# Kernel tuning notes

Hardware: AMD Instinct MI355X
Metric: run time of the kernel (lower is better)

Reference implementation:

```python
import jax, jax.numpy as jnp
import numpy as np

N = 10000   # nodes
E = 160000  # edges
IN_DIM, HID, OUT_DIM = 512, 512, 256


def setup_inputs() -> dict:
    key = jax.random.key(0)
    ks = jax.random.split(key, 10)
    x = jax.random.normal(ks[0], (N, IN_DIM), dtype=jnp.float32)
    edge_index = jax.random.randint(ks[1], (2, E), 0, N, dtype=jnp.int32)
    s = 0.05
    return {
        "x": x,
        "edge_index": edge_index,
        # GIN inner MLP (iVAE-style MLP with n_layers=1 == single Linear)
        "f_W": jax.random.normal(ks[2], (IN_DIM, HID), jnp.float32) * s,
        "f_b": jnp.zeros((HID,), jnp.float32),
        # GCNConv linear
        "gcn_W": jax.random.normal(ks[3], (IN_DIM + HID, OUT_DIM), jnp.float32) * s,
        "gcn_b": jnp.zeros((OUT_DIM,), jnp.float32),
        # decode MLP: out_dim -> out_dim/2 -> 2 with relu between
        "d1_W": jax.random.normal(ks[4], (OUT_DIM, OUT_DIM // 2), jnp.float32) * s,
        "d1_b": jnp.zeros((OUT_DIM // 2,), jnp.float32),
        "d2_W": jax.random.normal(ks[5], (OUT_DIM // 2, 2), jnp.float32) * s,
        "d2_b": jnp.zeros((2,), jnp.float32),
    }


def reference(x, edge_index, f_W, f_b, gcn_W, gcn_b, d1_W, d1_b, d2_W, d2_b):
    src, dst = edge_index[0], edge_index[1]

    # ---- GINConv(f, eps=-1.0): out = f((1+eps)*x + sum_{j in N(i)} x_j)
    # eps = -1 => (1+eps) = 0, so only the neighbor sum survives.
    agg = jax.ops.segment_sum(x[src], dst, num_segments=N)      # [N, in_dim]
    h1 = agg @ f_W + f_b                                        # [N, hid]

    # (the original computes z1 = (h1-mean)/std when regularize=True, but it is
    #  overwritten before being returned -> dead code, skipped)

    # ---- GCNConv on cat(x, h1) with self-loops + symmetric normalization
    xh = jnp.concatenate((x, h1), axis=1)                       # [N, in+hid]
    h = xh @ gcn_W                                              # [N, out]

    loop = jnp.arange(N, dtype=src.dtype)
    src_f = jnp.concatenate([src, loop])                        # [E+N]
    dst_f = jnp.concatenate([dst, loop])
    deg = jax.ops.segment_sum(jnp.ones_like(dst_f, jnp.float32), dst_f,
                              num_segments=N)                   # [N]
    dis = jnp.where(deg > 0, jax.lax.rsqrt(jnp.maximum(deg, 1.0)), 0.0)
    norm = dis[src_f] * dis[dst_f]                              # [E+N]
    out = jax.ops.segment_sum(h[src_f] * norm[:, None], dst_f,
                              num_segments=N) + gcn_b           # [N, out]

    # ---- decode MLP: Linear -> relu -> Linear
    z = jax.nn.relu(out @ d1_W + d1_b)
    z1 = z @ d2_W + d2_b                                        # [N, 2]
    return z1
```

## Files before the change

kernel.cpp:

```cpp
#include <hip/hip_runtime.h>

#define N_NODES 10000
#define E_EDGES 160000
#define IN_DIM  512
#define HID_DIM 512
#define OUT_DIM 256
#define MB_T    157

typedef __attribute__((ext_vector_type(8))) short short8;
typedef __attribute__((ext_vector_type(16))) float f32x16;
typedef unsigned short u16;

__device__ __forceinline__ u16 f2bh(float f) {
  union { float f; unsigned u; } v; v.f = f;
  return (u16)((v.u + 0x7FFFu + ((v.u >> 16) & 1u)) >> 16);
}
__device__ __forceinline__ float bh2f(u16 h) {
  union { unsigned u; float f; } v; v.u = ((unsigned)h) << 16;
  return v.f;
}

__device__ __forceinline__ size_t tidx(int mb, int ktTot, int kt, int c) {
  return ((size_t)(mb * ktTot + kt) * 256 + c) * 8;
}
__device__ __forceinline__ short8 g16(const u16* p) {
  return *reinterpret_cast<const short8*>(p);
}

#define GL_LDS(gsrc, ldst)                                                      \
  __builtin_amdgcn_global_load_lds(                                             \
      (const __attribute__((address_space(1))) unsigned int*)(gsrc),            \
      (__attribute__((address_space(3))) unsigned int*)(ldst), 16, 0, 0)

__global__ __launch_bounds__(1024) void scan_kernel(
    int* __restrict__ cnt, int* __restrict__ row, float* __restrict__ dis) {
  __shared__ int wsum[16];
  const int CH = 10;
  int t = threadIdx.x;
  int lane = t & 63, wid = t >> 6;
  int c[CH], excl[CH];
  int s = 0;
#pragma unroll
  for (int j = 0; j < CH; ++j) {
    int idx = t * CH + j;
    c[j] = (idx < N_NODES) ? cnt[idx] : 0;
    excl[j] = s;
    s += c[j];
  }
  int incl = s;
#pragma unroll
  for (int off = 1; off < 64; off <<= 1) {
    int v = __shfl_up(incl, off);
    if (lane >= off) incl += v;
  }
  if (lane == 63) wsum[wid] = incl;
  __syncthreads();
  if (t < 16) {
    int v = wsum[t];
#pragma unroll
    for (int off = 1; off < 16; off <<= 1) {
      int u = __shfl_up(v, off);
      if (t >= off) v += u;
    }
    wsum[t] = v;
  }
  __syncthreads();
  int waveBase = (wid == 0) ? 0 : wsum[wid - 1];
  int base = waveBase + incl - s;
#pragma unroll
  for (int j = 0; j < CH; ++j) {
    int idx = t * CH + j;
    if (idx < N_NODES) {
      int start = base + excl[j];
      row[idx] = start;
      cnt[idx] = start;
      dis[idx] = rsqrtf((float)c[j] + 1.0f);
    }
  }
  if (t == 1023) row[N_NODES] = wsum[15];
}

#define PREP_PACKX  5000
#define PREP_PACKFW 5256
#define PREP_CONVT  5320
#define PREP_C2END  5336
#define PREP_TOTAL  5961

__device__ __forceinline__ void pack_row(const float* __restrict__ src,
                                         u16* __restrict__ hi, u16* __restrict__ lo,
                                         int i, int tt) {
  int k0 = tt * 4;
  float4 v = *reinterpret_cast<const float4*>(src + (size_t)i * 512 + k0);
  float a[4] = {v.x, v.y, v.z, v.w};
  ushort4 h4, l4;
  u16* hp = &h4.x; u16* lp = &l4.x;
#pragma unroll
  for (int j = 0; j < 4; ++j) {
    u16 hh = f2bh(a[j]);
    hp[j] = hh;
    lp[j] = f2bh(a[j] - bh2f(hh));
  }
  int mb = i >> 6, rl = i & 63;
  int kt = k0 >> 5, si = (k0 >> 4) & 1, kh = (k0 >> 3) & 1;
  int c = (rl >> 5) * 128 + si * 64 + kh * 32 + (rl & 31);
  size_t idx = tidx(mb, 16, kt, c) + (k0 & 7);
  *reinterpret_cast<ushort4*>(hi + idx) = h4;
  *reinterpret_cast<ushort4*>(lo + idx) = l4;
}

__global__ __launch_bounds__(256) void prep_kernel(
    const float* __restrict__ x, const float* __restrict__ f_W,
    const float* __restrict__ gcn_W, const float* __restrict__ f_b,
    const int* __restrict__ dst, int* __restrict__ icnt,
    u16* __restrict__ x_hi, u16* __restrict__ x_lo,
    u16* __restrict__ fWp_hi, u16* __restrict__ fWp_lo,
    u16* __restrict__ Wcomb_hi, u16* __restrict__ Wcomb_lo,
    u16* __restrict__ WbotT_hi, u16* __restrict__ WbotT_lo,
    float* __restrict__ c2) {
  __shared__ float tile[64][65];
  int b = blockIdx.x, t = threadIdx.x;

  if (b < PREP_PACKX) {
    int i = b * 2 + (t >> 7);
    pack_row(x, x_hi, x_lo, i, t & 127);
  } else if (b < PREP_PACKFW) {
    int i = (b - PREP_PACKX) * 2 + (t >> 7);
    pack_row(f_W, fWp_hi, fWp_lo, i, t & 127);
  } else if (b < PREP_CONVT) {
    int lb = b - PREP_PACKFW;
    int part = lb >> 5;
    int li = lb & 31;
    int k0g = (li >> 2) * 64;
    int n0 = (li & 3) * 64;
    const float* W = part ? (gcn_W + (size_t)IN_DIM * OUT_DIM) : gcn_W;
    u16* hi = part ? WbotT_hi : Wcomb_hi;
    u16* lo = part ? WbotT_lo : Wcomb_lo;
    int lk = t >> 4, ln = (t & 15) * 4;
#pragma unroll
    for (int p = 0; p < 4; ++p) {
      float4 v = *reinterpret_cast<const float4*>(W + (size_t)(k0g + p * 16 + lk) * 256 + n0 + ln);
      tile[p * 16 + lk][ln + 0] = v.x;
      tile[p * 16 + lk][ln + 1] = v.y;
      tile[p * 16 + lk][ln + 2] = v.z;
      tile[p * 16 + lk][ln + 3] = v.w;
    }
    __syncthreads();
    int on = t >> 2;
    int ok = (t & 3) * 16;
    int colg = n0 + on;
    int nb = colg >> 6, rl = colg & 63;
#pragma unroll
    for (int q = 0; q < 4; ++q) {
      int kg = k0g + ok + q * 4;
      ushort4 h4, l4;
      u16* hq = &h4.x; u16* lq = &l4.x;
#pragma unroll
      for (int j = 0; j < 4; ++j) {
        float v = tile[ok + q * 4 + j][on];
        u16 hh = f2bh(v);
        hq[j] = hh;
        lq[j] = f2bh(v - bh2f(hh));
      }
      int kt = kg >> 5, si = (kg >> 4) & 1, kh = (kg >> 3) & 1;
      int c = (rl >> 5) * 128 + si * 64 + kh * 32 + (rl & 31);
      size_t idx = tidx(nb, 16, kt, c) + (kg & 7);
      *reinterpret_cast<ushort4*>(hi + idx) = h4;
      *reinterpret_cast<ushort4*>(lo + idx) = l4;
    }
  } else if (b < PREP_C2END) {
    int cb = b - PREP_CONVT;
    float s = 0.f;
    int kb = cb * 32;
#pragma unroll 8
    for (int k = kb; k < kb + 32; ++k)
      s += f_b[k] * gcn_W[(size_t)(IN_DIM + k) * OUT_DIM + t];
    atomicAdd(&c2[t], s);
  } else {
    int e = (b - PREP_C2END) * 256 + t;
    if (e < E_EDGES) atomicAdd(&icnt[dst[e]], 1);
  }
}

#define PW_PLACE 625
#define PW_TOTAL 657

__global__ __launch_bounds__(256) void pw_kernel(
    const int* __restrict__ src, const int* __restrict__ dst,
    int* __restrict__ cursor, int* __restrict__ col,
    const u16* __restrict__ WbotT_hi, const u16* __restrict__ WbotT_lo,
    const u16* __restrict__ fWp_hi, const u16* __restrict__ fWp_lo,
    u16* __restrict__ Wcomb_hi, u16* __restrict__ Wcomb_lo) {
  __shared__ u16 H[8192];
  int b = blockIdx.x, t = threadIdx.x;

  if (b < PW_PLACE) {
    int e = b * 256 + t;
    if (e < E_EDGES) {
      int pos = atomicAdd(&cursor[dst[e]], 1);
      col[pos] = src[e];
    }
    return;
  }

  int lb = b - PW_PLACE;
  int nb = lb & 7;
  int mbw = lb >> 3;
  int w = t >> 6, l = t & 63;
  int wr = w >> 1, wc = w & 1;
  int cA = wr * 128 + l;
  int cB = wc * 128 + l;

  f32x16 acc0, acc1;
#pragma unroll
  for (int r = 0; r < 16; ++r) { acc0[r] = 0.f; acc1[r] = 0.f; }

#define W2LOAD(KT, AH0, AL0, BH0, BL0, AH1, AL1, BH1, BL1)                     \
  {                                                                            \
    size_t a0 = tidx(mbw, 16, (KT), cA);                                       \
    size_t a1 = tidx(mbw, 16, (KT), cA + 64);                                  \
    size_t b0 = tidx(nb, 16, (KT), cB);                                        \
    size_t b1 = tidx(nb, 16, (KT), cB + 64);                                   \
    AH0 = g16(WbotT_hi + a0); AL0 = g16(WbotT_lo + a0);                        \
    BH0 = g16(fWp_hi + b0);   BL0 = g16(fWp_lo + b0);                          \
    AH1 = g16(WbotT_hi + a1); AL1 = g16(WbotT_lo + a1);                        \
    BH1 = g16(fWp_hi + b1);   BL1 = g16(fWp_lo + b1);                          \
  }
#define W2MMA(AH0, AL0, BH0, BL0, AH1, AL1, BH1, BL1)                          \
  {                                                                            \
    acc0 = __builtin_amdgcn_mfma_f32_32x32x16_bf16(AH0, BH0, acc0, 0, 0, 0);   \
    acc0 = __builtin_amdgcn_mfma_f32_32x32x16_bf16(AL0, BH0, acc0, 0, 0, 0);   \
    acc0 = __builtin_amdgcn_mfma_f32_32x32x16_bf16(AH0, BL0, acc0, 0, 0, 0);   \
    acc1 = __builtin_amdgcn_mfma_f32_32x32x16_bf16(AH1, BH1, acc1, 0, 0, 0);   \
    acc1 = __builtin_amdgcn_mfma_f32_32x32x16_bf16(AL1, BH1, acc1, 0, 0, 0);   \
    acc1 = __builtin_amdgcn_mfma_f32_32x32x16_bf16(AH1, BL1, acc1, 0, 0, 0);   \
  }

  short8 xah0, xal0, xbh0, xbl0, xah1, xal1, xbh1, xbl1;
  short8 yah0, yal0, ybh0, ybl0, yah1, yal1, ybh1, ybl1;
  W2LOAD(0, xah0, xal0, xbh0, xbl0, xah1, xal1, xbh1, xbl1)
#pragma unroll
  for (int kt = 0; kt < 16; kt += 2) {
    W2LOAD(kt + 1, yah0, yal0, ybh0, ybl0, yah1, yal1, ybh1, ybl1)
    W2MMA(xah0, xal0, xbh0, xbl0, xah1, xal1, xbh1, xbl1)
    if (kt + 2 < 16)
      W2LOAD(kt + 2, xah0, xal0, xbh0, xbl0, xah1, xal1, xbh1, xbl1)
    W2MMA(yah0, yal0, ybh0, ybl0, yah1, yal1, ybh1, ybl1)
  }
#undef W2LOAD
#undef W2MMA

  f32x16 acc = acc0 + acc1;
  u16* Hhi = H;
  u16* Hlo = H + 4096;
  int r0l = wr * 32 + 4 * (l >> 5);
  int c0l = wc * 32 + (l & 31);
#pragma unroll
  for (int r = 0; r < 16; ++r) {
    int rl = r0l + (r & 3) + 8 * (r >> 2);
    float v = acc[r];
    u16 hh = f2bh(v);
    Hhi[rl * 64 + c0l] = hh;
    Hlo[rl * 64 + c0l] = f2bh(v - bh2f(hh));
  }
  __syncthreads();
#pragma unroll
  for (int pl = 0; pl < 2; ++pl) {
    const u16* Hs = pl ? Hlo : Hhi;
    u16* dA = pl ? Wcomb_lo : Wcomb_hi;
#pragma unroll
    for (int j = 0; j < 2; ++j) {
      int ci = t + j * 256;
      int ktl = ci >> 8;
      int c = ci & 255;
      int r = ((c >> 7) & 1) * 32 + (c & 31);
      int kloc = ktl * 32 + ((c >> 6) & 1) * 16 + ((c >> 5) & 1) * 8;
      short8 v = *reinterpret_cast<const short8*>(Hs + r * 64 + kloc);
      size_t db = tidx(mbw + 4, 16, nb * 2 + ktl, c);
      *reinterpret_cast<short8*>(dA + db) = v;
    }
  }
}

template <int NB>
__global__ __launch_bounds__(256) void zgemm_kernel(
    const u16* __restrict__ Ah, const u16* __restrict__ Al,
    const u16* __restrict__ Bh, const u16* __restrict__ Bl,
    float* __restrict__ z1, u16* __restrict__ z2b, int M, int K) {
  constexpr int BCH = NB * 256;
  __shared__ short8 S[2][512 + 2 * BCH];

  int bid = blockIdx.x;
  int X = bid & 7, sslot = bid >> 3;
  int mb = X + 8 * (sslot >> 2);
  int nbB = sslot & 3;
  if (mb >= MB_T) return;

  int t = threadIdx.x, w = t >> 6, l = t & 63;
  int wr = w >> 1, wc = w & 1;
  int cid = t;
  int ktTot = K >> 5;

  f32x16 acc[NB][2];
#pragma unroll
  for (int n = 0; n < NB; ++n)
#pragma unroll
    for (int si = 0; si < 2; ++si)
#pragma unroll
      for (int r = 0; r < 16; ++r) acc[n][si][r] = 0.f;

  int nt = K / 32;

#define ZSTAGE(BUF, K0)                                                        \
  {                                                                            \
    size_t ab = tidx(mb, ktTot, (K0) >> 5, cid);                               \
    short8* base = &S[BUF][0] + w * 64;                                        \
    GL_LDS(Ah + ab, base);                                                     \
    GL_LDS(Al + ab, base + 256);                                               \
    _Pragma("unroll") for (int j = 0; j < NB; ++j) {                           \
      size_t bb = tidx(nbB * NB + j, ktTot, (K0) >> 5, cid);                   \
      GL_LDS(Bh + bb, base + 512 + j * 256);                                   \
      GL_LDS(Bl + bb, base + 512 + BCH + j * 256);                             \
    }                                                                          \
  }

  ZSTAGE(0, 0)
  for (int ti = 0; ti < nt; ++ti) {
    int b = ti & 1;
    __syncthreads();
    if (ti + 1 < nt) ZSTAGE(b ^ 1, (ti + 1) * 32)
#pragma unroll
    for (int si = 0; si < 2; ++si) {
      short8 ah = S[b][wr * 128 + si * 64 + l];
      short8 al = S[b][256 + wr * 128 + si * 64 + l];
#pragma unroll
      for (int n2 = 0; n2 < NB; ++n2) {
        short8 bh = S[b][512 + wc * 256 + n2 * 128 + si * 64 + l];
        short8 bl = S[b][512 + BCH + wc * 256 + n2 * 128 + si * 64 + l];
        acc[n2][si] = __builtin_amdgcn_mfma_f32_32x32x16_bf16(ah, bh, acc[n2][si], 0, 0, 0);
        acc[n2][si] = __builtin_amdgcn_mfma_f32_32x32x16_bf16(al, bh, acc[n2][si], 0, 0, 0);
        acc[n2][si] = __builtin_amdgcn_mfma_f32_32x32x16_bf16(ah, bl, acc[n2][si], 0, 0, 0);
      }
    }
  }
#undef ZSTAGE

  int r0 = mb * 64 + wr * 32 + 4 * (l >> 5);
#pragma unroll
  for (int n2 = 0; n2 < NB; ++n2) {
    f32x16 a = acc[n2][0] + acc[n2][1];
    int colg = nbB * (NB * 64) + wc * 64 + n2 * 32 + (l & 31);
#pragma unroll
    for (int r = 0; r < 16; ++r) {
      int rowg = r0 + (r & 3) + 8 * (r >> 2);
      if (rowg < M) {
        float v = a[r];
        if (colg < 256) z1[(size_t)rowg * 256 + colg] = v;
        else            z2b[(size_t)rowg * 256 + colg - 256] = f2bh(v);
      }
    }
  }
}

__global__ __launch_bounds__(128) void h_build_kernel(
    const float* __restrict__ z1, const u16* __restrict__ z2b,
    const int* __restrict__ row, const int* __restrict__ col,
    const float* __restrict__ c2, float* __restrict__ h,
    u16* __restrict__ h_bf) {
  int i = blockIdx.x * 2 + (threadIdx.x >> 6);
  int t = threadIdx.x & 63;
  int half = t >> 5, sl = t & 31;
  int beg = row[i], end = row[i + 1];

  float a0[8] = {}, a1[8] = {}, a2[8] = {}, a3[8] = {};
  int e = beg + half;
  for (; e + 6 < end; e += 8) {
    int s0 = col[e], s1 = col[e + 2], s2 = col[e + 4], s3 = col[e + 6];
    short8 v0 = *reinterpret_cast<const short8*>(z2b + (size_t)s0 * 256 + sl * 8);
    short8 v1 = *reinterpret_cast<const short8*>(z2b + (size_t)s1 * 256 + sl * 8);
    short8 v2 = *reinterpret_cast<const short8*>(z2b + (size_t)s2 * 256 + sl * 8);
    short8 v3 = *reinterpret_cast<const short8*>(z2b + (size_t)s3 * 256 + sl * 8);
#pragma unroll
    for (int j = 0; j < 8; ++j) {
      a0[j] += bh2f((u16)v0[j]);
      a1[j] += bh2f((u16)v1[j]);
      a2[j] += bh2f((u16)v2[j]);
      a3[j] += bh2f((u16)v3[j]);
    }
  }
  for (; e < end; e += 2) {
    int s = col[e];
    short8 v = *reinterpret_cast<const short8*>(z2b + (size_t)s * 256 + sl * 8);
#pragma unroll
    for (int j = 0; j < 8; ++j) a0[j] += bh2f((u16)v[j]);
  }
  float acc[8];
#pragma unroll
  for (int j = 0; j < 8; ++j) {
    acc[j] = a0[j] + a1[j] + a2[j] + a3[j];
    acc[j] += __shfl_xor(acc[j], 32);
  }
  float4 z1a = *reinterpret_cast<const float4*>(z1 + (size_t)i * 256 + sl * 8);
  float4 z1b = *reinterpret_cast<const float4*>(z1 + (size_t)i * 256 + sl * 8 + 4);
  float4 ca = *reinterpret_cast<const float4*>(c2 + sl * 8);
  float4 cb = *reinterpret_cast<const float4*>(c2 + sl * 8 + 4);
  float hv[8] = {z1a.x + ca.x + acc[0], z1a.y + ca.y + acc[1],
                 z1a.z + ca.z + acc[2], z1a.w + ca.w + acc[3],
                 z1b.x + cb.x + acc[4], z1b.y + cb.y + acc[5],
                 z1b.z + cb.z + acc[6], z1b.w + cb.w + acc[7]};
  if (half == 0) {
    float4 o0{hv[0], hv[1], hv[2], hv[3]};
    float4 o1{hv[4], hv[5], hv[6], hv[7]};
    *reinterpret_cast<float4*>(h + (size_t)i * 256 + sl * 8) = o0;
    *reinterpret_cast<float4*>(h + (size_t)i * 256 + sl * 8 + 4) = o1;
    short8 hb;
#pragma unroll
    for (int j = 0; j < 8; ++j) hb[j] = (short)f2bh(hv[j]);
    *reinterpret_cast<short8*>(h_bf + (size_t)i * 256 + sl * 8) = hb;
  }
}

__global__ __launch_bounds__(128) void gcn_gather_kernel(
    const float* __restrict__ h, const u16* __restrict__ h_bf,
    const int* __restrict__ row, const int* __restrict__ col,
    const float* __restrict__ dis, const float* __restrict__ gcn_b,
    float* __restrict__ outg) {
  int i = blockIdx.x * 2 + (threadIdx.x >> 6);
  int t = threadIdx.x & 63;
  int half = t >> 5, sl = t & 31;
  int beg = row[i], end = row[i + 1];
  float di = dis[i];

  float a0[8] = {}, a1[8] = {}, a2[8] = {}, a3[8] = {};
  int e = beg + half;
  for (; e + 6 < end; e += 8) {
    int s0 = col[e], s1 = col[e + 2], s2 = col[e + 4], s3 = col[e + 6];
    float w0 = dis[s0], w1 = dis[s1], w2 = dis[s2], w3 = dis[s3];
    short8 v0 = *reinterpret_cast<const short8*>(h_bf + (size_t)s0 * 256 + sl * 8);
    short8 v1 = *reinterpret_cast<const short8*>(h_bf + (size_t)s1 * 256 + sl * 8);
    short8 v2 = *reinterpret_cast<const short8*>(h_bf + (size_t)s2 * 256 + sl * 8);
    short8 v3 = *reinterpret_cast<const short8*>(h_bf + (size_t)s3 * 256 + sl * 8);
#pragma unroll
    for (int j = 0; j < 8; ++j) {
      a0[j] += w0 * bh2f((u16)v0[j]);
      a1[j] += w1 * bh2f((u16)v1[j]);
      a2[j] += w2 * bh2f((u16)v2[j]);
      a3[j] += w3 * bh2f((u16)v3[j]);
    }
  }
  for (; e < end; e += 2) {
    int s = col[e];
    float wv = dis[s];
    short8 v = *reinterpret_cast<const short8*>(h_bf + (size_t)s * 256 + sl * 8);
#pragma unroll
    for (int j = 0; j < 8; ++j) a0[j] += wv * bh2f((u16)v[j]);
  }
  float acc[8];
#pragma unroll
  for (int j = 0; j < 8; ++j) {
    acc[j] = a0[j] + a1[j] + a2[j] + a3[j];
    acc[j] += __shfl_xor(acc[j], 32);
  }
  if (half == 0) {
    float4 ha = *reinterpret_cast<const float4*>(h + (size_t)i * 256 + sl * 8);
    float4 hb = *reinterpret_cast<const float4*>(h + (size_t)i * 256 + sl * 8 + 4);
    float4 ba = *reinterpret_cast<const float4*>(gcn_b + sl * 8);
    float4 bb = *reinterpret_cast<const float4*>(gcn_b + sl * 8 + 4);
    float self = di * di;
    float4 o0{di * acc[0] + self * ha.x + ba.x, di * acc[1] + self * ha.y + ba.y,
              di * acc[2] + self * ha.z + ba.z, di * acc[3] + self * ha.w + ba.w};
    float4 o1{di * acc[4] + self * hb.x + bb.x, di * acc[5] + self * hb.y + bb.y,
              di * acc[6] + self * hb.z + bb.z, di * acc[7] + self * hb.w + bb.w};
    *reinterpret_cast<float4*>(outg + (size_t)i * 256 + sl * 8) = o0;
    *reinterpret_cast<float4*>(outg + (size_t)i * 256 + sl * 8 + 4) = o1;
  }
}

#define DEC_NODES 8
__global__ __launch_bounds__(128) void decode_kernel(
    const float* __restrict__ outg, const float* __restrict__ d1_W,
    const float* __restrict__ d1_b, const float* __restrict__ d2_W,
    const float* __restrict__ d2_b, float* __restrict__ z1) {
  __shared__ float rows[DEC_NODES][OUT_DIM];
  __shared__ float s0[128], s1[128];
  int t = threadIdx.x;
  int n0 = blockIdx.x * DEC_NODES;
#pragma unroll
  for (int j = 0; j < 4; ++j) {
    int idx = j * 512 + t * 4;
    *reinterpret_cast<float4*>(&rows[0][idx]) =
        *reinterpret_cast<const float4*>(outg + (size_t)n0 * OUT_DIM + idx);
  }
  __syncthreads();
  float acc[DEC_NODES];
  float b1 = d1_b[t];
#pragma unroll
  for (int n = 0; n < DEC_NODES; ++n) acc[n] = b1;
#pragma unroll 4
  for (int k = 0; k < OUT_DIM; ++k) {
    float wv = d1_W[k * 128 + t];
#pragma unroll
    for (int n = 0; n < DEC_NODES; ++n) acc[n] += rows[n][k] * wv;
  }
  float w0 = d2_W[t * 2 + 0], w1 = d2_W[t * 2 + 1];
  for (int n = 0; n < DEC_NODES; ++n) {
    float a = fmaxf(acc[n], 0.f);
    s0[t] = a * w0;
    s1[t] = a * w1;
    __syncthreads();
    for (int off = 64; off > 0; off >>= 1) {
      if (t < off) {
        s0[t] += s0[t + off];
        s1[t] += s1[t + off];
      }
      __syncthreads();
    }
    if (t == 0) {
      z1[(size_t)(n0 + n) * 2 + 0] = s0[0] + d2_b[0];
      z1[(size_t)(n0 + n) * 2 + 1] = s1[0] + d2_b[1];
    }
    __syncthreads();
  }
}

extern "C" void kernel_launch(void* const* d_in, const int* in_sizes, int n_in,
                              void* d_out, int out_size, void* d_ws, size_t ws_size,
                              hipStream_t stream) {
  const float* x     = (const float*)d_in[0];
  const int*   edge  = (const int*)d_in[1];
  const float* f_W   = (const float*)d_in[2];
  const float* f_b   = (const float*)d_in[3];
  const float* gcn_W = (const float*)d_in[4];
  const float* gcn_b = (const float*)d_in[5];
  const float* d1_W  = (const float*)d_in[6];
  const float* d1_b  = (const float*)d_in[7];
  const float* d2_W  = (const float*)d_in[8];
  const float* d2_b  = (const float*)d_in[9];
  float* out = (float*)d_out;
  char*  wsb = (char*)d_ws;

  const int* src = edge;
  const int* dst = edge + E_EDGES;

  const size_t TS   = (size_t)MB_T * 16 * 256 * 8 * sizeof(u16);
  const size_t WTLE = (size_t)16 * 256 * 8 * sizeof(u16);

  size_t o = 0;
  u16*   x_hi = (u16*)(wsb + o); o += TS;
  u16*   x_lo = (u16*)(wsb + o); o += TS;
  float* z1   = (float*)(wsb + o); o += (size_t)N_NODES * 256 * 4;
  u16*   z2b  = (u16*)(wsb + o);   o += (size_t)N_NODES * 256 * 2;
  float* h    = (float*)(wsb + o); o += (size_t)N_NODES * 256 * 4;
  u16*   h_bf = (u16*)(wsb + o);   o += (size_t)N_NODES * 256 * 2;
  float* dis8 = (float*)(wsb + o); o += (size_t)N_NODES * 4;
  int*   icnt8 = (int*)(wsb + o);  o += (size_t)N_NODES * 4;
  float* c2   = (float*)(wsb + o); o += OUT_DIM * 4;
  int*   irow8 = (int*)(wsb + o);  o += (size_t)(N_NODES + 1) * 4 + 12;
  int*   icol8 = (int*)(wsb + o);  o += (size_t)E_EDGES * 4;
  u16*   Wcomb_hi = (u16*)(wsb + o); o += 8 * WTLE;
  u16*   Wcomb_lo = (u16*)(wsb + o); o += 8 * WTLE;
  u16*   WbotT_hi = (u16*)(wsb + o); o += 4 * WTLE;
  u16*   WbotT_lo = (u16*)(wsb + o); o += 4 * WTLE;
  u16*   fWp_hi   = (u16*)(wsb + o); o += 8 * WTLE;
  u16*   fWp_lo   = (u16*)(wsb + o); o += 8 * WTLE;
  float* outg = (float*)(wsb + 0);
  const size_t v8_needed = o;

  if (ws_size >= v8_needed) {
    hipMemsetAsync(icnt8, 0, (size_t)N_NODES * sizeof(int) + OUT_DIM * sizeof(float), stream);

    prep_kernel<<<PREP_TOTAL, 256, 0, stream>>>(
        x, f_W, gcn_W, f_b, dst, icnt8, x_hi, x_lo, fWp_hi, fWp_lo,
        Wcomb_hi, Wcomb_lo, WbotT_hi, WbotT_lo, c2);

    scan_kernel<<<1, 1024, 0, stream>>>(icnt8, irow8, dis8);

    pw_kernel<<<PW_TOTAL, 256, 0, stream>>>(
        src, dst, icnt8, icol8, WbotT_hi, WbotT_lo, fWp_hi, fWp_lo,
        Wcomb_hi, Wcomb_lo);

    zgemm_kernel<2><<<640, 256, 0, stream>>>(
        x_hi, x_lo, Wcomb_hi, Wcomb_lo, z1, z2b, N_NODES, IN_DIM);

    h_build_kernel<<<N_NODES / 2, 128, 0, stream>>>(z1, z2b, irow8, icol8, c2, h, h_bf);

    gcn_gather_kernel<<<N_NODES / 2, 128, 0, stream>>>(h, h_bf, irow8, icol8, dis8, gcn_b, outg);
    decode_kernel<<<N_NODES / DEC_NODES, 128, 0, stream>>>(outg, d1_W, d1_b, d2_W, d2_b, out);
  }
}
```

Baseline: 142.5 us.

## Split bf16 gather tables into column halves for L2-resident neighbor gathers

```diff
diff --git a/kernel.cpp b/kernel.cpp
--- a/kernel.cpp
+++ b/kernel.cpp
@@ -285,7 +285,8 @@
 __global__ __launch_bounds__(256) void zgemm_kernel(
     const u16* __restrict__ Ah, const u16* __restrict__ Al,
     const u16* __restrict__ Bh, const u16* __restrict__ Bl,
-    float* __restrict__ z1, u16* __restrict__ z2b, int M, int K) {
+    float* __restrict__ z1, u16* __restrict__ z2A, u16* __restrict__ z2B,
+    int M, int K) {
   constexpr int BCH = NB * 256;
   __shared__ short8 S[2][512 + 2 * BCH];
 
@@ -354,124 +355,142 @@
       int rowg = r0 + (r & 3) + 8 * (r >> 2);
       if (rowg < M) {
         float v = a[r];
-        if (colg < 256) z1[(size_t)rowg * 256 + colg] = v;
-        else            z2b[(size_t)rowg * 256 + colg - 256] = f2bh(v);
+        if (colg < 256) {
+          z1[(size_t)rowg * 256 + colg] = v;
+        } else {
+          int cg = colg - 256;
+          u16* dp = (cg < 128) ? z2A : z2B;
+          dp[(size_t)rowg * 128 + (cg & 127)] = f2bh(v);
+        }
       }
     }
   }
 }
 
 __global__ __launch_bounds__(128) void h_build_kernel(
-    const float* __restrict__ z1, const u16* __restrict__ z2b,
-    const int* __restrict__ row, const int* __restrict__ col,
-    const float* __restrict__ c2, float* __restrict__ h,
-    u16* __restrict__ h_bf) {
+    const float* __restrict__ z1, const u16* __restrict__ z2A,
+    const u16* __restrict__ z2B, const int* __restrict__ row,
+    const int* __restrict__ col, const float* __restrict__ c2,
+    float* __restrict__ h, u16* __restrict__ hbA, u16* __restrict__ hbB) {
   int i = blockIdx.x * 2 + (threadIdx.x >> 6);
   int t = threadIdx.x & 63;
-  int half = t >> 5, sl = t & 31;
+  int q = t >> 4, sl = t & 15;
   int beg = row[i], end = row[i + 1];
 
-  float a0[8] = {}, a1[8] = {}, a2[8] = {}, a3[8] = {};
-  int e = beg + half;
-  for (; e + 6 < end; e += 8) {
-    int s0 = col[e], s1 = col[e + 2], s2 = col[e + 4], s3 = col[e + 6];
-    short8 v0 = *reinterpret_cast<const short8*>(z2b + (size_t)s0 * 256 + sl * 8);
-    short8 v1 = *reinterpret_cast<const short8*>(z2b + (size_t)s1 * 256 + sl * 8);
-    short8 v2 = *reinterpret_cast<const short8*>(z2b + (size_t)s2 * 256 + sl * 8);
-    short8 v3 = *reinterpret_cast<const short8*>(z2b + (size_t)s3 * 256 + sl * 8);
+#pragma unroll
+  for (int half = 0; half < 2; ++half) {
+    const u16* z2 = half ? z2B : z2A;
+    u16* hb = half ? hbB : hbA;
+    float a0[8] = {}, a1[8] = {}, a2[8] = {}, a3[8] = {};
+    int e = beg + q;
+    for (; e + 12 < end; e += 16) {
+      int s0 = col[e], s1 = col[e + 4], s2 = col[e + 8], s3 = col[e + 12];
+      short8 v0 = g16(z2 + (size_t)s0 * 128 + sl * 8);
+      short8 v1 = g16(z2 + (size_t)s1 * 128 + sl * 8);
+      short8 v2 = g16(z2 + (size_t)s2 * 128 + sl * 8);
+      short8 v3 = g16(z2 + (size_t)s3 * 128 + sl * 8);
+#pragma unroll
+      for (int j = 0; j < 8; ++j) {
+        a0[j] += bh2f((u16)v0[j]);
+        a1[j] += bh2f((u16)v1[j]);
+        a2[j] += bh2f((u16)v2[j]);
+        a3[j] += bh2f((u16)v3[j]);
+      }
+    }
+    for (; e < end; e += 4) {
+      int s = col[e];
+      short8 v = g16(z2 + (size_t)s * 128 + sl * 8);
+#pragma unroll
+      for (int j = 0; j < 8; ++j) a0[j] += bh2f((u16)v[j]);
+    }
+    float acc[8];
 #pragma unroll
     for (int j = 0; j < 8; ++j) {
-      a0[j] += bh2f((u16)v0[j]);
-      a1[j] += bh2f((u16)v1[j]);
-      a2[j] += bh2f((u16)v2[j]);
-      a3[j] += bh2f((u16)v3[j]);
-    }
-  }
-  for (; e < end; e += 2) {
-    int s = col[e];
-    short8 v = *reinterpret_cast<const short8*>(z2b + (size_t)s * 256 + sl * 8);
-#pragma unroll
-    for (int j = 0; j < 8; ++j) a0[j] += bh2f((u16)v[j]);
-  }
-  float acc[8];
-#pragma unroll
-  for (int j = 0; j < 8; ++j) {
-    acc[j] = a0[j] + a1[j] + a2[j] + a3[j];
-    acc[j] += __shfl_xor(acc[j], 32);
-  }
-  float4 z1a = *reinterpret_cast<const float4*>(z1 + (size_t)i * 256 + sl * 8);
-  float4 z1b = *reinterpret_cast<const float4*>(z1 + (size_t)i * 256 + sl * 8 + 4);
-  float4 ca = *reinterpret_cast<const float4*>(c2 + sl * 8);
-  float4 cb = *reinterpret_cast<const float4*>(c2 + sl * 8 + 4);
-  float hv[8] = {z1a.x + ca.x + acc[0], z1a.y + ca.y + acc[1],
-                 z1a.z + ca.z + acc[2], z1a.w + ca.w + acc[3],
-                 z1b.x + cb.x + acc[4], z1b.y + cb.y + acc[5],
-                 z1b.z + cb.z + acc[6], z1b.w + cb.w + acc[7]};
-  if (half == 0) {
-    float4 o0{hv[0], hv[1], hv[2], hv[3]};
-    float4 o1{hv[4], hv[5], hv[6], hv[7]};
-    *reinterpret_cast<float4*>(h + (size_t)i * 256 + sl * 8) = o0;
-    *reinterpret_cast<float4*>(h + (size_t)i * 256 + sl * 8 + 4) = o1;
-    short8 hb;
-#pragma unroll
-    for (int j = 0; j < 8; ++j) hb[j] = (short)f2bh(hv[j]);
-    *reinterpret_cast<short8*>(h_bf + (size_t)i * 256 + sl * 8) = hb;
+      acc[j] = a0[j] + a1[j] + a2[j] + a3[j];
+      acc[j] += __shfl_xor(acc[j], 16);
+      acc[j] += __shfl_xor(acc[j], 32);
+    }
+    if (t < 16) {
+      size_t base = (size_t)i * 256 + half * 128 + sl * 8;
+      float4 za = *reinterpret_cast<const float4*>(z1 + base);
+      float4 zb = *reinterpret_cast<const float4*>(z1 + base + 4);
+      float4 ca = *reinterpret_cast<const float4*>(c2 + half * 128 + sl * 8);
+      float4 cb = *reinterpret_cast<const float4*>(c2 + half * 128 + sl * 8 + 4);
+      float hv[8] = {za.x + ca.x + acc[0], za.y + ca.y + acc[1],
+                     za.z + ca.z + acc[2], za.w + ca.w + acc[3],
+                     zb.x + cb.x + acc[4], zb.y + cb.y + acc[5],
+                     zb.z + cb.z + acc[6], zb.w + cb.w + acc[7]};
+      float4 o0{hv[0], hv[1], hv[2], hv[3]};
+      float4 o1{hv[4], hv[5], hv[6], hv[7]};
+      *reinterpret_cast<float4*>(h + base) = o0;
+      *reinterpret_cast<float4*>(h + base + 4) = o1;
+      short8 hb8;
+#pragma unroll
+      for (int j = 0; j < 8; ++j) hb8[j] = (short)f2bh(hv[j]);
+      *reinterpret_cast<short8*>(hb + (size_t)i * 128 + sl * 8) = hb8;
+    }
   }
 }
 
 __global__ __launch_bounds__(128) void gcn_gather_kernel(
-    const float* __restrict__ h, const u16* __restrict__ h_bf,
-    const int* __restrict__ row, const int* __restrict__ col,
-    const float* __restrict__ dis, const float* __restrict__ gcn_b,
-    float* __restrict__ outg) {
+    const float* __restrict__ h, const u16* __restrict__ hbA,
+    const u16* __restrict__ hbB, const int* __restrict__ row,
+    const int* __restrict__ col, const float* __restrict__ dis,
+    const float* __restrict__ gcn_b, float* __restrict__ outg) {
   int i = blockIdx.x * 2 + (threadIdx.x >> 6);
   int t = threadIdx.x & 63;
-  int half = t >> 5, sl = t & 31;
+  int q = t >> 4, sl = t & 15;
   int beg = row[i], end = row[i + 1];
   float di = dis[i];
 
-  float a0[8] = {}, a1[8] = {}, a2[8] = {}, a3[8] = {};
-  int e = beg + half;
-  for (; e + 6 < end; e += 8) {
-    int s0 = col[e], s1 = col[e + 2], s2 = col[e + 4], s3 = col[e + 6];
-    float w0 = dis[s0], w1 = dis[s1], w2 = dis[s2], w3 = dis[s3];
-    short8 v0 = *reinterpret_cast<const short8*>(h_bf + (size_t)s0 * 256 + sl * 8);
-    short8 v1 = *reinterpret_cast<const short8*>(h_bf + (size_t)s1 * 256 + sl * 8);
-    short8 v2 = *reinterpret_cast<const short8*>(h_bf + (size_t)s2 * 256 + sl * 8);
-    short8 v3 = *reinterpret_cast<const short8*>(h_bf + (size_t)s3 * 256 + sl * 8);
+#pragma unroll
+  for (int half = 0; half < 2; ++half) {
+    const u16* hb = half ? hbB : hbA;
+    float a0[8] = {}, a1[8] = {}, a2[8] = {}, a3[8] = {};
+    int e = beg + q;
+    for (; e + 12 < end; e += 16) {
+      int s0 = col[e], s1 = col[e + 4], s2 = col[e + 8], s3 = col[e + 12];
+      float w0 = dis[s0], w1 = dis[s1], w2 = dis[s2], w3 = dis[s3];
+      short8 v0 = g16(hb + (size_t)s0 * 128 + sl * 8);
+      short8 v1 = g16(hb + (size_t)s1 * 128 + sl * 8);
+      short8 v2 = g16(hb + (size_t)s2 * 128 + sl * 8);
+      short8 v3 = g16(hb + (size_t)s3 * 128 + sl * 8);
+#pragma unroll
+      for (int j = 0; j < 8; ++j) {
+        a0[j] += w0 * bh2f((u16)v0[j]);
+        a1[j] += w1 * bh2f((u16)v1[j]);
+        a2[j] += w2 * bh2f((u16)v2[j]);
+        a3[j] += w3 * bh2f((u16)v3[j]);
+      }
+    }
+    for (; e < end; e += 4) {
+      int s = col[e];
+      float wv = dis[s];
+      short8 v = g16(hb + (size_t)s * 128 + sl * 8);
+#pragma unroll
+      for (int j = 0; j < 8; ++j) a0[j] += wv * bh2f((u16)v[j]);
+    }
+    float acc[8];
 #pragma unroll
     for (int j = 0; j < 8; ++j) {
-      a0[j] += w0 * bh2f((u16)v0[j]);
-      a1[j] += w1 * bh2f((u16)v1[j]);
-      a2[j] += w2 * bh2f((u16)v2[j]);
-      a3[j] += w3 * bh2f((u16)v3[j]);
-    }
-  }
-  for (; e < end; e += 2) {
-    int s = col[e];
-    float wv = dis[s];
-    short8 v = *reinterpret_cast<const short8*>(h_bf + (size_t)s * 256 + sl * 8);
-#pragma unroll
-    for (int j = 0; j < 8; ++j) a0[j] += wv * bh2f((u16)v[j]);
-  }
-  float acc[8];
-#pragma unroll
-  for (int j = 0; j < 8; ++j) {
-    acc[j] = a0[j] + a1[j] + a2[j] + a3[j];
-    acc[j] += __shfl_xor(acc[j], 32);
-  }
-  if (half == 0) {
-    float4 ha = *reinterpret_cast<const float4*>(h + (size_t)i * 256 + sl * 8);
-    float4 hb = *reinterpret_cast<const float4*>(h + (size_t)i * 256 + sl * 8 + 4);
-    float4 ba = *reinterpret_cast<const float4*>(gcn_b + sl * 8);
-    float4 bb = *reinterpret_cast<const float4*>(gcn_b + sl * 8 + 4);
-    float self = di * di;
-    float4 o0{di * acc[0] + self * ha.x + ba.x, di * acc[1] + self * ha.y + ba.y,
-              di * acc[2] + self * ha.z + ba.z, di * acc[3] + self * ha.w + ba.w};
-    float4 o1{di * acc[4] + self * hb.x + bb.x, di * acc[5] + self * hb.y + bb.y,
-              di * acc[6] + self * hb.z + bb.z, di * acc[7] + self * hb.w + bb.w};
-    *reinterpret_cast<float4*>(outg + (size_t)i * 256 + sl * 8) = o0;
-    *reinterpret_cast<float4*>(outg + (size_t)i * 256 + sl * 8 + 4) = o1;
+      acc[j] = a0[j] + a1[j] + a2[j] + a3[j];
+      acc[j] += __shfl_xor(acc[j], 16);
+      acc[j] += __shfl_xor(acc[j], 32);
+    }
+    if (t < 16) {
+      size_t base = (size_t)i * 256 + half * 128 + sl * 8;
+      float4 ha = *reinterpret_cast<const float4*>(h + base);
+      float4 hb4 = *reinterpret_cast<const float4*>(h + base + 4);
+      float4 ba = *reinterpret_cast<const float4*>(gcn_b + half * 128 + sl * 8);
+      float4 bb = *reinterpret_cast<const float4*>(gcn_b + half * 128 + sl * 8 + 4);
+      float self = di * di;
+      float4 o0{di * acc[0] + self * ha.x + ba.x, di * acc[1] + self * ha.y + ba.y,
+                di * acc[2] + self * ha.z + ba.z, di * acc[3] + self * ha.w + ba.w};
+      float4 o1{di * acc[4] + self * hb4.x + bb.x, di * acc[5] + self * hb4.y + bb.y,
+                di * acc[6] + self * hb4.z + bb.z, di * acc[7] + self * hb4.w + bb.w};
+      *reinterpret_cast<float4*>(outg + base) = o0;
+      *reinterpret_cast<float4*>(outg + base + 4) = o1;
+    }
   }
 }
 
@@ -548,14 +567,16 @@
   u16*   x_hi = (u16*)(wsb + o); o += TS;
   u16*   x_lo = (u16*)(wsb + o); o += TS;
   float* z1   = (float*)(wsb + o); o += (size_t)N_NODES * 256 * 4;
-  u16*   z2b  = (u16*)(wsb + o);   o += (size_t)N_NODES * 256 * 2;
+  u16*   z2A  = (u16*)(wsb + o);   o += (size_t)N_NODES * 128 * 2;
+  u16*   z2B  = (u16*)(wsb + o);   o += (size_t)N_NODES * 128 * 2;
   float* h    = (float*)(wsb + o); o += (size_t)N_NODES * 256 * 4;
-  u16*   h_bf = (u16*)(wsb + o);   o += (size_t)N_NODES * 256 * 2;
-  float* dis8 = (float*)(wsb + o); o += (size_t)N_NODES * 4;
-  int*   icnt8 = (int*)(wsb + o);  o += (size_t)N_NODES * 4;
+  u16*   hbA  = (u16*)(wsb + o);   o += (size_t)N_NODES * 128 * 2;
+  u16*   hbB  = (u16*)(wsb + o);   o += (size_t)N_NODES * 128 * 2;
+  float* dis9 = (float*)(wsb + o); o += (size_t)N_NODES * 4;
+  int*   icnt9 = (int*)(wsb + o);  o += (size_t)N_NODES * 4;
   float* c2   = (float*)(wsb + o); o += OUT_DIM * 4;
-  int*   irow8 = (int*)(wsb + o);  o += (size_t)(N_NODES + 1) * 4 + 12;
-  int*   icol8 = (int*)(wsb + o);  o += (size_t)E_EDGES * 4;
+  int*   irow9 = (int*)(wsb + o);  o += (size_t)(N_NODES + 1) * 4 + 12;
+  int*   icol9 = (int*)(wsb + o);  o += (size_t)E_EDGES * 4;
   u16*   Wcomb_hi = (u16*)(wsb + o); o += 8 * WTLE;
   u16*   Wcomb_lo = (u16*)(wsb + o); o += 8 * WTLE;
   u16*   WbotT_hi = (u16*)(wsb + o); o += 4 * WTLE;
@@ -563,27 +584,30 @@
   u16*   fWp_hi   = (u16*)(wsb + o); o += 8 * WTLE;
   u16*   fWp_lo   = (u16*)(wsb + o); o += 8 * WTLE;
   float* outg = (float*)(wsb + 0);
-  const size_t v8_needed = o;
-
-  if (ws_size >= v8_needed) {
-    hipMemsetAsync(icnt8, 0, (size_t)N_NODES * sizeof(int) + OUT_DIM * sizeof(float), stream);
+  const size_t v9_needed = o;
+
+  if (ws_size >= v9_needed) {
+    hipMemsetAsync(icnt9, 0, (size_t)N_NODES * sizeof(int) + OUT_DIM * sizeof(float), stream);
 
     prep_kernel<<<PREP_TOTAL, 256, 0, stream>>>(
-        x, f_W, gcn_W, f_b, dst, icnt8, x_hi, x_lo, fWp_hi, fWp_lo,
+        x, f_W, gcn_W, f_b, dst, icnt9, x_hi, x_lo, fWp_hi, fWp_lo,
         Wcomb_hi, Wcomb_lo, WbotT_hi, WbotT_lo, c2);
 
-    scan_kernel<<<1, 1024, 0, stream>>>(icnt8, irow8, dis8);
+    scan_kernel<<<1, 1024, 0, stream>>>(icnt9, irow9, dis9);
 
     pw_kernel<<<PW_TOTAL, 256, 0, stream>>>(
-        src, dst, icnt8, icol8, WbotT_hi, WbotT_lo, fWp_hi, fWp_lo,
+        src, dst, icnt9, icol9, WbotT_hi, WbotT_lo, fWp_hi, fWp_lo,
         Wcomb_hi, Wcomb_lo);
 
     zgemm_kernel<2><<<640, 256, 0, stream>>>(
-        x_hi, x_lo, Wcomb_hi, Wcomb_lo, z1, z2b, N_NODES, IN_DIM);
-
-    h_build_kernel<<<N_NODES / 2, 128, 0, stream>>>(z1, z2b, irow8, icol8, c2, h, h_bf);
-
-    gcn_gather_kernel<<<N_NODES / 2, 128, 0, stream>>>(h, h_bf, irow8, icol8, dis8, gcn_b, outg);
-    decode_kernel<<<N_NODES / DEC_NODES, 128, 0, stream>>>(outg, d1_W, d1_b, d2_W, d2_b, out);
-  }
-}
+        x_hi, x_lo, Wcomb_hi, Wcomb_lo, z1, z2A, z2B, N_NODES, IN_DIM);
+
+    h_build_kernel<<<N_NODES / 2, 128, 0, stream>>>(
+        z1, z2A, z2B, irow9, icol9, c2, h, hbA, hbB);
+
+    gcn_gather_kernel<<<N_NODES / 2, 128, 0, stream>>>(
+        h, hbA, hbB, irow9, icol9, dis9, gcn_b, outg);
+    decode_kernel<<<N_NODES / DEC_NODES, 128, 0, stream>>>(
+        outg, d1_W, d1_b, d2_W, d2_b, out);
+  }
+}
```

Result: slower. 149.7 us (+5.1%).
